# Optimization experiments

Hardware: AMD Instinct MI355X
Metric: run time of the kernel (lower is better)

The kernel has to match this reference:

```python
import jax, jax.numpy as jnp
import numpy as np

D = 1024  # in_features == latent_dim
EPS = 1e-5


def _layernorm(x, g, b):
    mu = jnp.mean(x, axis=-1, keepdims=True)
    var = jnp.mean(jnp.square(x - mu), axis=-1, keepdims=True)
    return (x - mu) * jax.lax.rsqrt(var + EPS) * g + b


def setup_inputs() -> dict:
    key = jax.random.key(0)
    ks = jax.random.split(key, 8)
    s = 1.0 / np.sqrt(D)
    return {
        "x": jax.random.normal(ks[0], (4, 4096, D), dtype=jnp.float32),
        "w_qkv": jax.random.uniform(ks[1], (3 * D, D), jnp.float32, -s, s),
        "w_o": jax.random.uniform(ks[2], (D, D), jnp.float32, -s, s),
        "w1": jax.random.uniform(ks[3], (D, D), jnp.float32, -s, s),
        "b1": jax.random.uniform(ks[4], (D,), jnp.float32, -s, s),
        "w2": jax.random.uniform(ks[5], (D, D), jnp.float32, -s, s),
        "b2": jax.random.uniform(ks[6], (D,), jnp.float32, -s, s),
        "ln1_g": jnp.ones((D,), jnp.float32),
        "ln1_b": jnp.zeros((D,), jnp.float32),
        "ln2_g": jnp.ones((D,), jnp.float32),
        "ln2_b": jnp.zeros((D,), jnp.float32),
    }


def reference(x, w_qkv, w_o, w1, b1, w2, b2, ln1_g, ln1_b, ln2_g, ln2_b):
    B, S, _ = x.shape
    scale = 1.0 / np.sqrt(D * 1)  # 1/sqrt(latent_dim * n_heads), n_heads=1
    qkv = jnp.einsum("bsd,ed->bse", x, w_qkv)            # [B,S,3D]
    qkv = qkv.reshape(B, S, 1, 3 * D).transpose(0, 2, 1, 3)  # [B,1,S,3D]
    q, k, v = jnp.split(qkv, 3, axis=-1)                  # each [B,1,S,D]
    logits = jnp.einsum("bhid,bhjd->bhij", q, k) * scale  # [B,1,S,S]
    # Faithful quirk: softmax over the HEAD axis (dim=1). With 1 head this
    # yields an all-ones attention matrix.
    attn = jax.nn.softmax(logits, axis=1)
    vals = jnp.einsum("bhij,bhjd->bhid", attn, v)         # [B,1,S,D]
    vals = vals.transpose(0, 2, 1, 3).reshape(B, S, D)
    attn_out = jnp.einsum("bsd,ed->bse", vals, w_o)
    # squeeze(-2) is a no-op for S>1
    x = _layernorm(x + attn_out, ln1_g, ln1_b)
    h = jax.nn.gelu(jnp.einsum("bsd,ed->bse", x, w1) + b1, approximate=False)
    mlp_out = jnp.einsum("bsd,ed->bse", h, w2) + b2
    return _layernorm(x + mlp_out, ln2_g, ln2_b)
```

## Files before the change

kernel.cpp:

```cpp
#include <hip/hip_runtime.h>
#include <hip/hip_bf16.h>

typedef __hip_bfloat16 bf16;
typedef __attribute__((ext_vector_type(8))) short short8;
typedef __attribute__((ext_vector_type(4))) float f32x4;

#define DDIM 1024
#define SEQ  4096
#define NB   4
#define MTOT (NB*SEQ)

static __device__ __forceinline__ unsigned short f2bf(float f) {
    __hip_bfloat16 h = __float2bfloat16(f);
    unsigned short u; __builtin_memcpy(&u, &h, 2); return u;
}
static __device__ __forceinline__ float bf2f(unsigned short u) {
    __hip_bfloat16 h; __builtin_memcpy(&h, &u, 2); return __bfloat162float(h);
}

__global__ __launch_bounds__(256) void cast_w_kernel(
    const float* __restrict__ w1, const float* __restrict__ w2,
    unsigned short* __restrict__ w1b, unsigned short* __restrict__ w2b)
{
    size_t idx = ((size_t)blockIdx.x*256 + threadIdx.x) * 4;
    float4 a = *(const float4*)(w1 + idx);
    ushort4 o; o.x=f2bf(a.x); o.y=f2bf(a.y); o.z=f2bf(a.z); o.w=f2bf(a.w);
    *(ushort4*)(w1b + idx) = o;
    float4 b = *(const float4*)(w2 + idx);
    o.x=f2bf(b.x); o.y=f2bf(b.y); o.z=f2bf(b.z); o.w=f2bf(b.w);
    *(ushort4*)(w2b + idx) = o;
}

__global__ __launch_bounds__(256) void colsum_partial_kernel(
    const float* __restrict__ x, float* __restrict__ partial)
{
    int d  = blockIdx.x*256 + threadIdx.x;
    int b  = blockIdx.y;
    int sl = blockIdx.z;
    const float* p = x + ((size_t)b*SEQ + (size_t)sl*128)*DDIM + d;
    float s = 0.f;
    #pragma unroll 4
    for (int i = 0; i < 128; ++i) s += p[(size_t)i*DDIM];
    partial[((size_t)sl*NB + b)*DDIM + d] = s;
}

__global__ __launch_bounds__(256) void colsum_reduce_kernel(
    const float* __restrict__ partial, float* __restrict__ xsum)
{
    int d = blockIdx.x*256 + threadIdx.x;
    int b = blockIdx.y;
    float s = 0.f;
    #pragma unroll
    for (int sl = 0; sl < 32; ++sl) s += partial[((size_t)sl*NB + b)*DDIM + d];
    xsum[b*DDIM + d] = s;
}

__global__ __launch_bounds__(256) void matvec_kernel(
    const float* __restrict__ W, const float* __restrict__ vin, float* __restrict__ vout)
{
    int b = blockIdx.y;
    int g = threadIdx.x >> 4;
    int t = threadIdx.x & 15;
    int e = blockIdx.x*16 + g;
    const float* w = W + (size_t)e*DDIM;
    const float* v = vin + b*DDIM;
    float s = 0.f;
    for (int k = t; k < DDIM; k += 16) s += w[k]*v[k];
    #pragma unroll
    for (int o = 8; o; o >>= 1) s += __shfl_down(s, o, 16);
    if (t == 0) vout[b*DDIM + e] = s;
}

__global__ __launch_bounds__(256) void ln1_kernel(
    const float* __restrict__ x, const float* __restrict__ avec,
    const float* __restrict__ g1, const float* __restrict__ b1,
    unsigned short* __restrict__ x1b)
{
    int row = blockIdx.x;
    int b   = row >> 12;
    int tid = threadIdx.x;
    const float4* xr = (const float4*)(x + (size_t)row*DDIM);
    const float4* av = (const float4*)(avec + (size_t)b*DDIM);
    float4 xv = xr[tid], a4 = av[tid];
    float y0 = xv.x+a4.x, y1 = xv.y+a4.y, y2 = xv.z+a4.z, y3 = xv.w+a4.w;
    float s  = y0+y1+y2+y3;
    float ss = y0*y0+y1*y1+y2*y2+y3*y3;
    #pragma unroll
    for (int o = 32; o; o >>= 1) { s += __shfl_down(s,o,64); ss += __shfl_down(ss,o,64); }
    __shared__ float red[8];
    if ((tid&63) == 0) { red[tid>>6] = s; red[4+(tid>>6)] = ss; }
    __syncthreads();
    float St = red[0]+red[1]+red[2]+red[3];
    float Sq = red[4]+red[5]+red[6]+red[7];
    float mu = St*(1.0f/DDIM);
    float rs = rsqrtf(Sq*(1.0f/DDIM) - mu*mu + 1e-5f);
    float4 g4 = ((const float4*)g1)[tid];
    float4 bb = ((const float4*)b1)[tid];
    ushort4 o;
    o.x = f2bf((y0-mu)*rs*g4.x + bb.x);
    o.y = f2bf((y1-mu)*rs*g4.y + bb.y);
    o.z = f2bf((y2-mu)*rs*g4.z + bb.z);
    o.w = f2bf((y3-mu)*rs*g4.w + bb.w);
    *(ushort4*)(x1b + (size_t)row*DDIM + tid*4) = o;
}

template<int MODE>
__global__ __launch_bounds__(256, 2) void gemm128_kernel(
    const bf16* __restrict__ A, const bf16* __restrict__ Bw,
    const float* __restrict__ bias, const unsigned short* __restrict__ resid,
    unsigned short* __restrict__ outb, float* __restrict__ outf)
{
    constexpr int K = 1024, N = 1024, BK = 64, NT = K / BK;
    __shared__ __align__(16) bf16 lds[2][2][128*BK];
    const int tid  = threadIdx.x;
    const int wave = tid >> 6, lane = tid & 63;

    int bid = blockIdx.x;
    int swz = (bid & 7) * 128 + (bid >> 3);
    const size_t bm = (size_t)(swz >> 3) * 128;
    const size_t bn = (size_t)(swz & 7) * 128;

    const int wm = wave >> 1;
    const int wn = wave & 1;

    const int srow = tid >> 3;
    const int skel = (((tid & 7) ^ ((tid >> 3) & 7)) << 3);

    const int frow = lane & 15;
    int foff[2];
    #pragma unroll
    for (int ks = 0; ks < 2; ++ks)
        foff[ks] = frow*128 + (((ks*4 + (lane >> 4)) ^ (lane & 7)) << 4);

    f32x4 acc[4][4] = {};
    const bf16* Ab = A  + bm * K;
    const bf16* Bb = Bw + bn * K;

    auto stage = [&](int b, int kt) {
        #pragma unroll
        for (int mat = 0; mat < 2; ++mat) {
            const bf16* src = (mat == 0 ? Ab : Bb);
            #pragma unroll
            for (int g = 0; g < 4; ++g) {
                int row = g*32 + srow;
                const bf16* gp = src + (size_t)row * K + kt*BK + skel;
                __builtin_amdgcn_global_load_lds(
                    (const __attribute__((address_space(1))) void*)gp,
                    (__attribute__((address_space(3))) void*)
                        ((char*)&lds[b][mat][0] + g*4096 + wave*1024),
                    16, 0, 0);
            }
        }
    };

    stage(0, 0);

    #pragma unroll 2
    for (int t = 0; t < NT; ++t) {
        const int cur = t & 1;
        if (t < NT-1) {
            stage(cur ^ 1, t + 1);
            asm volatile("s_waitcnt vmcnt(8)" ::: "memory");
        } else {
            asm volatile("s_waitcnt vmcnt(0)" ::: "memory");
        }
        __builtin_amdgcn_s_barrier();

        const char* LA = (const char*)&lds[cur][0][0] + wm*8192;
        const char* LB = (const char*)&lds[cur][1][0] + wn*8192;
        #pragma unroll
        for (int ks = 0; ks < 2; ++ks) {
            short8 af[4], bfr[4];
            #pragma unroll
            for (int m = 0; m < 4; ++m) af[m]  = *(const short8*)(LA + m*2048 + foff[ks]);
            #pragma unroll
            for (int n = 0; n < 4; ++n) bfr[n] = *(const short8*)(LB + n*2048 + foff[ks]);
            __builtin_amdgcn_s_setprio(1);
            #pragma unroll
            for (int m = 0; m < 4; ++m)
                #pragma unroll
                for (int n = 0; n < 4; ++n)
                    acc[m][n] = __builtin_amdgcn_mfma_f32_16x16x32_bf16(af[m], bfr[n], acc[m][n], 0, 0, 0);
            __builtin_amdgcn_s_setprio(0);
        }
        __builtin_amdgcn_s_barrier();
    }

    const int crow = (lane >> 4) * 4, ccol = lane & 15;
    #pragma unroll
    for (int n = 0; n < 4; ++n) {
        size_t col = bn + wn*64 + n*16 + ccol;
        float bv = bias[col];
        #pragma unroll
        for (int m = 0; m < 4; ++m) {
            #pragma unroll
            for (int r = 0; r < 4; ++r) {
                size_t row = bm + wm*64 + m*16 + crow + r;
                float v = acc[m][n][r] + bv;
                if (MODE == 1) {
                    float ge = 0.5f*v*(1.0f + erff(v*0.70710678118f));
                    outb[row*(size_t)N + col] = f2bf(ge);
                } else {
                    outf[row*(size_t)N + col] = v + bf2f(resid[row*(size_t)N + col]);
                }
            }
        }
    }
}

__global__ __launch_bounds__(256) void ln2_kernel(
    float* __restrict__ out, const float* __restrict__ g2, const float* __restrict__ b2)
{
    int row = blockIdx.x;
    int tid = threadIdx.x;
    float4* orow = (float4*)(out + (size_t)row*DDIM);
    float4 y = orow[tid];
    float s  = y.x+y.y+y.z+y.w;
    float ss = y.x*y.x+y.y*y.y+y.z*y.z+y.w*y.w;
    #pragma unroll
    for (int o = 32; o; o >>= 1) { s += __shfl_down(s,o,64); ss += __shfl_down(ss,o,64); }
    __shared__ float red[8];
    if ((tid&63) == 0) { red[tid>>6] = s; red[4+(tid>>6)] = ss; }
    __syncthreads();
    float St = red[0]+red[1]+red[2]+red[3];
    float Sq = red[4]+red[5]+red[6]+red[7];
    float mu = St*(1.0f/DDIM);
    float rs = rsqrtf(Sq*(1.0f/DDIM) - mu*mu + 1e-5f);
    float4 g4 = ((const float4*)g2)[tid];
    float4 bb = ((const float4*)b2)[tid];
    float4 n;
    n.x = (y.x-mu)*rs*g4.x + bb.x;
    n.y = (y.y-mu)*rs*g4.y + bb.y;
    n.z = (y.z-mu)*rs*g4.z + bb.z;
    n.w = (y.w-mu)*rs*g4.w + bb.w;
    orow[tid] = n;
}

extern "C" void kernel_launch(void* const* d_in, const int* in_sizes, int n_in,
                              void* d_out, int out_size, void* d_ws, size_t ws_size,
                              hipStream_t stream)
{
    const float* x     = (const float*)d_in[0];
    const float* w_qkv = (const float*)d_in[1];
    const float* w_o   = (const float*)d_in[2];
    const float* w1    = (const float*)d_in[3];
    const float* b1    = (const float*)d_in[4];
    const float* w2    = (const float*)d_in[5];
    const float* b2    = (const float*)d_in[6];
    const float* ln1g  = (const float*)d_in[7];
    const float* ln1b  = (const float*)d_in[8];
    const float* ln2g  = (const float*)d_in[9];
    const float* ln2b  = (const float*)d_in[10];
    float* out = (float*)d_out;
    char* ws = (char*)d_ws;

    unsigned short* x1b = (unsigned short*)(ws);
    unsigned short* hb  = (unsigned short*)(ws + 33554432);
    unsigned short* w1b = (unsigned short*)(ws + 67108864);
    unsigned short* w2b = (unsigned short*)(ws + 69206016);
    float* partial = (float*)(ws + 71303168);
    float* xsum    = (float*)(ws + 71827456);
    float* tvec    = (float*)(ws + 71843840);
    float* avec    = (float*)(ws + 71860224);

    cast_w_kernel<<<dim3(1024), 256, 0, stream>>>(w1, w2, w1b, w2b);
    colsum_partial_kernel<<<dim3(4, NB, 32), 256, 0, stream>>>(x, partial);
    colsum_reduce_kernel<<<dim3(4, NB), 256, 0, stream>>>(partial, xsum);
    matvec_kernel<<<dim3(64, NB), 256, 0, stream>>>(w_qkv + (size_t)2*DDIM*DDIM, xsum, tvec);
    matvec_kernel<<<dim3(64, NB), 256, 0, stream>>>(w_o, tvec, avec);
    ln1_kernel<<<dim3(MTOT), 256, 0, stream>>>(x, avec, ln1g, ln1b, x1b);
    gemm128_kernel<1><<<dim3(1024), 256, 0, stream>>>(
        (const bf16*)x1b, (const bf16*)w1b, b1, nullptr, hb, nullptr);
    gemm128_kernel<2><<<dim3(1024), 256, 0, stream>>>(
        (const bf16*)hb, (const bf16*)w2b, b2, x1b, nullptr, out);
    ln2_kernel<<<dim3(MTOT), 256, 0, stream>>>(out, ln2g, ln2b);
}
```

Baseline: 174.6 us.

## Pre-pack weights into MFMA fragment layout and load B directly to registers

The weight cast kernel now writes w1/w2 as bf16 in MFMA B-fragment order, so each lane can fetch its 16-byte fragment with one coalesced global load. The GEMM keeps only A in LDS through global_load_lds, and B fragments are double-buffered in registers and prefetched one k-step ahead. This halves LDS traffic and the LDS footprint and removes the B LDS reads. In exchange each wave loads its own B fragments, so B global and L2 traffic rises because the two wm waves duplicate them, and register pressure increases.

```diff
diff --git a/kernel.cpp b/kernel.cpp
--- a/kernel.cpp
+++ b/kernel.cpp
@@ -18,17 +18,24 @@
     __hip_bfloat16 h; __builtin_memcpy(&h, &u, 2); return __bfloat162float(h);
 }
 
-__global__ __launch_bounds__(256) void cast_w_kernel(
+__global__ __launch_bounds__(256) void pack_w_kernel(
     const float* __restrict__ w1, const float* __restrict__ w2,
-    unsigned short* __restrict__ w1b, unsigned short* __restrict__ w2b)
-{
-    size_t idx = ((size_t)blockIdx.x*256 + threadIdx.x) * 4;
-    float4 a = *(const float4*)(w1 + idx);
-    ushort4 o; o.x=f2bf(a.x); o.y=f2bf(a.y); o.z=f2bf(a.z); o.w=f2bf(a.w);
-    *(ushort4*)(w1b + idx) = o;
-    float4 b = *(const float4*)(w2 + idx);
-    o.x=f2bf(b.x); o.y=f2bf(b.y); o.z=f2bf(b.z); o.w=f2bf(b.w);
-    *(ushort4*)(w2b + idx) = o;
+    short8* __restrict__ w1p, short8* __restrict__ w2p)
+{
+    int gid  = blockIdx.x*256 + threadIdx.x;
+    int m    = gid >> 17;
+    int id   = gid & 131071;
+    int frag = id >> 6, lane = id & 63;
+    int ntile = frag >> 5, kt32 = frag & 31;
+    int n = ntile*16 + (lane & 15);
+    int k = kt32*32 + (lane >> 4)*8;
+    const float* src = (m ? w2 : w1) + (size_t)n*DDIM + k;
+    float4 a = *(const float4*)src;
+    float4 b = *(const float4*)(src + 4);
+    short8 o;
+    o[0]=(short)f2bf(a.x); o[1]=(short)f2bf(a.y); o[2]=(short)f2bf(a.z); o[3]=(short)f2bf(a.w);
+    o[4]=(short)f2bf(b.x); o[5]=(short)f2bf(b.y); o[6]=(short)f2bf(b.z); o[7]=(short)f2bf(b.w);
+    (m ? w2p : w1p)[id] = o;
 }
 
 __global__ __launch_bounds__(256) void colsum_partial_kernel(
@@ -105,13 +112,13 @@
 }
 
 template<int MODE>
-__global__ __launch_bounds__(256, 2) void gemm128_kernel(
-    const bf16* __restrict__ A, const bf16* __restrict__ Bw,
+__global__ __launch_bounds__(256, 2) void gemm_bp_kernel(
+    const bf16* __restrict__ A, const short8* __restrict__ Bp,
     const float* __restrict__ bias, const unsigned short* __restrict__ resid,
     unsigned short* __restrict__ outb, float* __restrict__ outf)
 {
     constexpr int K = 1024, N = 1024, BK = 64, NT = K / BK;
-    __shared__ __align__(16) bf16 lds[2][2][128*BK];
+    __shared__ __align__(16) bf16 lds[2][128*BK];
     const int tid  = threadIdx.x;
     const int wave = tid >> 6, lane = tid & 63;
 
@@ -126,64 +133,75 @@
     const int srow = tid >> 3;
     const int skel = (((tid & 7) ^ ((tid >> 3) & 7)) << 3);
 
-    const int frow = lane & 15;
+    const int fr = lane & 15;
+    const int fs = lane >> 4;
     int foff[2];
     #pragma unroll
     for (int ks = 0; ks < 2; ++ks)
-        foff[ks] = frow*128 + (((ks*4 + (lane >> 4)) ^ (lane & 7)) << 4);
+        foff[ks] = fr*128 + (((ks*4 + fs) ^ (fr & 7)) << 4);
+
+    const bf16* Ab = A + bm * K;
+    const int nt0 = (int)(bn >> 4) + wn*4;
+
+    auto stageA = [&](int b, int kt) {
+        #pragma unroll
+        for (int g = 0; g < 4; ++g) {
+            const bf16* gp = Ab + (size_t)(g*32 + srow) * K + kt*BK + skel;
+            __builtin_amdgcn_global_load_lds(
+                (const __attribute__((address_space(1))) void*)gp,
+                (__attribute__((address_space(3))) void*)
+                    ((char*)&lds[b][0] + g*4096 + wave*1024),
+                16, 0, 0);
+        }
+    };
+    auto loadB = [&](int kt, short8* bf_) {
+        #pragma unroll
+        for (int kk = 0; kk < 2; ++kk)
+            #pragma unroll
+            for (int nf = 0; nf < 4; ++nf)
+                bf_[kk*4 + nf] = Bp[((nt0 + nf)*32 + kt*2 + kk)*64 + lane];
+    };
 
     f32x4 acc[4][4] = {};
-    const bf16* Ab = A  + bm * K;
-    const bf16* Bb = Bw + bn * K;
-
-    auto stage = [&](int b, int kt) {
-        #pragma unroll
-        for (int mat = 0; mat < 2; ++mat) {
-            const bf16* src = (mat == 0 ? Ab : Bb);
-            #pragma unroll
-            for (int g = 0; g < 4; ++g) {
-                int row = g*32 + srow;
-                const bf16* gp = src + (size_t)row * K + kt*BK + skel;
-                __builtin_amdgcn_global_load_lds(
-                    (const __attribute__((address_space(1))) void*)gp,
-                    (__attribute__((address_space(3))) void*)
-                        ((char*)&lds[b][mat][0] + g*4096 + wave*1024),
-                    16, 0, 0);
-            }
-        }
-    };
-
-    stage(0, 0);
-
-    #pragma unroll 2
-    for (int t = 0; t < NT; ++t) {
-        const int cur = t & 1;
+    short8 bcur[8], bnxt[8];
+
+    stageA(0, 0);
+    loadB(0, bcur);
+
+    auto iter = [&](int t, short8* bc, short8* bn_) {
         if (t < NT-1) {
-            stage(cur ^ 1, t + 1);
-            asm volatile("s_waitcnt vmcnt(8)" ::: "memory");
+            stageA((t+1) & 1, t+1);
+            asm volatile("s_waitcnt vmcnt(4)" ::: "memory");
         } else {
             asm volatile("s_waitcnt vmcnt(0)" ::: "memory");
         }
         __builtin_amdgcn_s_barrier();
-
-        const char* LA = (const char*)&lds[cur][0][0] + wm*8192;
-        const char* LB = (const char*)&lds[cur][1][0] + wn*8192;
+        if (t < NT-1) {
+            loadB(t+1, bn_);
+            asm volatile("" ::: "memory");
+        }
+        const char* LA = (const char*)&lds[t & 1][0] + wm*8192;
         #pragma unroll
         for (int ks = 0; ks < 2; ++ks) {
-            short8 af[4], bfr[4];
-            #pragma unroll
-            for (int m = 0; m < 4; ++m) af[m]  = *(const short8*)(LA + m*2048 + foff[ks]);
-            #pragma unroll
-            for (int n = 0; n < 4; ++n) bfr[n] = *(const short8*)(LB + n*2048 + foff[ks]);
+            short8 af[4];
+            #pragma unroll
+            for (int m = 0; m < 4; ++m) af[m] = *(const short8*)(LA + m*2048 + foff[ks]);
             __builtin_amdgcn_s_setprio(1);
             #pragma unroll
             for (int m = 0; m < 4; ++m)
                 #pragma unroll
                 for (int n = 0; n < 4; ++n)
-                    acc[m][n] = __builtin_amdgcn_mfma_f32_16x16x32_bf16(af[m], bfr[n], acc[m][n], 0, 0, 0);
+                    acc[m][n] = __builtin_amdgcn_mfma_f32_16x16x32_bf16(
+                        af[m], bc[ks*4 + n], acc[m][n], 0, 0, 0);
             __builtin_amdgcn_s_setprio(0);
         }
         __builtin_amdgcn_s_barrier();
+    };
+
+    #pragma unroll
+    for (int t = 0; t < NT; t += 2) {
+        iter(t,   bcur, bnxt);
+        iter(t+1, bnxt, bcur);
     }
 
     const int crow = (lane >> 4) * 4, ccol = lane & 15;
@@ -256,22 +274,22 @@
 
     unsigned short* x1b = (unsigned short*)(ws);
     unsigned short* hb  = (unsigned short*)(ws + 33554432);
-    unsigned short* w1b = (unsigned short*)(ws + 67108864);
-    unsigned short* w2b = (unsigned short*)(ws + 69206016);
+    short8* w1p = (short8*)(ws + 67108864);
+    short8* w2p = (short8*)(ws + 69206016);
     float* partial = (float*)(ws + 71303168);
     float* xsum    = (float*)(ws + 71827456);
     float* tvec    = (float*)(ws + 71843840);
     float* avec    = (float*)(ws + 71860224);
 
-    cast_w_kernel<<<dim3(1024), 256, 0, stream>>>(w1, w2, w1b, w2b);
+    pack_w_kernel<<<dim3(1024), 256, 0, stream>>>(w1, w2, w1p, w2p);
     colsum_partial_kernel<<<dim3(4, NB, 32), 256, 0, stream>>>(x, partial);
     colsum_reduce_kernel<<<dim3(4, NB), 256, 0, stream>>>(partial, xsum);
     matvec_kernel<<<dim3(64, NB), 256, 0, stream>>>(w_qkv + (size_t)2*DDIM*DDIM, xsum, tvec);
     matvec_kernel<<<dim3(64, NB), 256, 0, stream>>>(w_o, tvec, avec);
     ln1_kernel<<<dim3(MTOT), 256, 0, stream>>>(x, avec, ln1g, ln1b, x1b);
-    gemm128_kernel<1><<<dim3(1024), 256, 0, stream>>>(
-        (const bf16*)x1b, (const bf16*)w1b, b1, nullptr, hb, nullptr);
-    gemm128_kernel<2><<<dim3(1024), 256, 0, stream>>>(
-        (const bf16*)hb, (const bf16*)w2b, b2, x1b, nullptr, out);
+    gemm_bp_kernel<1><<<dim3(1024), 256, 0, stream>>>(
+        (const bf16*)x1b, w1p, b1, nullptr, hb, nullptr);
+    gemm_bp_kernel<2><<<dim3(1024), 256, 0, stream>>>(
+        (const bf16*)hb, w2p, b2, x1b, nullptr, out);
     ln2_kernel<<<dim3(MTOT), 256, 0, stream>>>(out, ln2g, ln2b);
 }
```

After: 187.2 us. 7.2% more time.

## Fuse LN2 statistics into second GEMM epilogue and add single-buffered first GEMM

Applied to the files above, without the earlier changes.

The second GEMM's epilogue now writes the residual sum in bf16 in place over x1b and computes per-row partial sum and sum-of-squares through shuffles and LDS. It writes these partials to a small buffer, so the final LayerNorm kernel reads bf16 values plus 8 partials instead of re-reading and reducing an fp32 row. The first GEMM is replaced by a single-buffered BK=32 kernel with 3 blocks per CU that synchronises every k-step. This cuts fp32 traffic and a reduction pass, at the cost of rounding the pre-LN2 sum to bf16 and computing variance as E[x²]−mu² from bf16-rounded values. The lnpart buffer reuses the w1b region, which is safe because the first GEMM has finished reading it by then.

```diff
diff --git a/kernel.cpp b/kernel.cpp
--- a/kernel.cpp
+++ b/kernel.cpp
@@ -104,11 +104,84 @@
     *(ushort4*)(x1b + (size_t)row*DDIM + tid*4) = o;
 }
 
-template<int MODE>
-__global__ __launch_bounds__(256, 2) void gemm128_kernel(
+__global__ __launch_bounds__(256, 3) void gemm_s32_kernel(
     const bf16* __restrict__ A, const bf16* __restrict__ Bw,
-    const float* __restrict__ bias, const unsigned short* __restrict__ resid,
-    unsigned short* __restrict__ outb, float* __restrict__ outf)
+    const float* __restrict__ bias, unsigned short* __restrict__ outb)
+{
+    constexpr int K = 1024, N = 1024, BK = 32;
+    __shared__ __align__(16) bf16 As[128*BK];
+    __shared__ __align__(16) bf16 Bs[128*BK];
+    const int tid  = threadIdx.x;
+    const int wave = tid >> 6, lane = tid & 63;
+
+    int bid = blockIdx.x;
+    int swz = (bid & 7) * 128 + (bid >> 3);
+    const size_t bm = (size_t)(swz >> 3) * 128;
+    const size_t bn = (size_t)(swz & 7) * 128;
+
+    const int wr = (wave >> 1) * 64, wc = (wave & 1) * 64;
+    const int fr = lane & 15, fs = lane >> 4;
+
+    const int srow = lane >> 2;
+    const int sk   = (((lane & 3) ^ ((lane >> 3) & 3)) << 3);
+
+    const int swo = (fs ^ ((fr >> 1) & 3)) << 4;
+
+    f32x4 acc[4][4] = {};
+    const bf16* Ab = A  + bm * K;
+    const bf16* Bb = Bw + bn * K;
+
+    for (int kt = 0; kt < K; kt += BK) {
+        #pragma unroll
+        for (int c = 0; c < 2; ++c) {
+            int chunk = c*4 + wave;
+            const bf16* ga = Ab + (size_t)(chunk*16 + srow)*K + kt + sk;
+            const bf16* gb = Bb + (size_t)(chunk*16 + srow)*K + kt + sk;
+            __builtin_amdgcn_global_load_lds(
+                (const __attribute__((address_space(1))) void*)ga,
+                (__attribute__((address_space(3))) void*)((char*)As + chunk*1024), 16, 0, 0);
+            __builtin_amdgcn_global_load_lds(
+                (const __attribute__((address_space(1))) void*)gb,
+                (__attribute__((address_space(3))) void*)((char*)Bs + chunk*1024), 16, 0, 0);
+        }
+        __syncthreads();
+        short8 af[4], bfr[4];
+        #pragma unroll
+        for (int m = 0; m < 4; ++m) af[m]  = *(const short8*)((char*)As + (wr + m*16 + fr)*64 + swo);
+        #pragma unroll
+        for (int n = 0; n < 4; ++n) bfr[n] = *(const short8*)((char*)Bs + (wc + n*16 + fr)*64 + swo);
+        __builtin_amdgcn_s_setprio(1);
+        #pragma unroll
+        for (int m = 0; m < 4; ++m)
+            #pragma unroll
+            for (int n = 0; n < 4; ++n)
+                acc[m][n] = __builtin_amdgcn_mfma_f32_16x16x32_bf16(af[m], bfr[n], acc[m][n], 0, 0, 0);
+        __builtin_amdgcn_s_setprio(0);
+        __syncthreads();
+    }
+
+    const int crow = fs * 4, ccol = fr;
+    #pragma unroll
+    for (int n = 0; n < 4; ++n) {
+        size_t col = bn + wc + n*16 + ccol;
+        float bv = bias[col];
+        #pragma unroll
+        for (int m = 0; m < 4; ++m) {
+            #pragma unroll
+            for (int r = 0; r < 4; ++r) {
+                size_t row = bm + wr + m*16 + crow + r;
+                float v = acc[m][n][r] + bv;
+                float ge = 0.5f*v*(1.0f + erff(v*0.70710678118f));
+                outb[row*(size_t)N + col] = f2bf(ge);
+            }
+        }
+    }
+}
+
+__global__ __launch_bounds__(256, 2) void gemm2_kernel(
+    const bf16* __restrict__ A, const bf16* __restrict__ Bw,
+    const float* __restrict__ bias, unsigned short* __restrict__ xy,
+    float2* __restrict__ part)
 {
     constexpr int K = 1024, N = 1024, BK = 64, NT = K / BK;
     __shared__ __align__(16) bf16 lds[2][2][128*BK];
@@ -126,11 +199,12 @@
     const int srow = tid >> 3;
     const int skel = (((tid & 7) ^ ((tid >> 3) & 7)) << 3);
 
-    const int frow = lane & 15;
+    const int fr = lane & 15;
+    const int fs = lane >> 4;
     int foff[2];
     #pragma unroll
     for (int ks = 0; ks < 2; ++ks)
-        foff[ks] = frow*128 + (((ks*4 + (lane >> 4)) ^ (lane & 7)) << 4);
+        foff[ks] = fr*128 + (((ks*4 + fs) ^ (fr & 7)) << 4);
 
     f32x4 acc[4][4] = {};
     const bf16* Ab = A  + bm * K;
@@ -180,60 +254,86 @@
             for (int m = 0; m < 4; ++m)
                 #pragma unroll
                 for (int n = 0; n < 4; ++n)
-                    acc[m][n] = __builtin_amdgcn_mfma_f32_16x16x32_bf16(af[m], bfr[n], acc[m][n], 0, 0, 0);
+                    acc[m][n] = __builtin_amdgcn_mfma_f32_16x16x32_bf16(
+                        af[m], bfr[n], acc[m][n], 0, 0, 0);
             __builtin_amdgcn_s_setprio(0);
         }
         __builtin_amdgcn_s_barrier();
     }
 
-    const int crow = (lane >> 4) * 4, ccol = lane & 15;
+    float vs[4][4] = {}, vq[4][4] = {};
     #pragma unroll
     for (int n = 0; n < 4; ++n) {
-        size_t col = bn + wn*64 + n*16 + ccol;
+        size_t col = bn + wn*64 + n*16 + fr;
         float bv = bias[col];
         #pragma unroll
         for (int m = 0; m < 4; ++m) {
             #pragma unroll
             for (int r = 0; r < 4; ++r) {
-                size_t row = bm + wm*64 + m*16 + crow + r;
-                float v = acc[m][n][r] + bv;
-                if (MODE == 1) {
-                    float ge = 0.5f*v*(1.0f + erff(v*0.70710678118f));
-                    outb[row*(size_t)N + col] = f2bf(ge);
-                } else {
-                    outf[row*(size_t)N + col] = v + bf2f(resid[row*(size_t)N + col]);
-                }
-            }
-        }
-    }
-}
-
-__global__ __launch_bounds__(256) void ln2_kernel(
-    float* __restrict__ out, const float* __restrict__ g2, const float* __restrict__ b2)
+                size_t row = bm + wm*64 + m*16 + fs*4 + r;
+                size_t idx = row*(size_t)N + col;
+                float v = acc[m][n][r] + bv + bf2f(xy[idx]);
+                unsigned short qb = f2bf(v);
+                xy[idx] = qb;
+                float vv = bf2f(qb);
+                vs[m][r] += vv;
+                vq[m][r] += vv*vv;
+            }
+        }
+    }
+    #pragma unroll
+    for (int o = 1; o < 16; o <<= 1) {
+        #pragma unroll
+        for (int m = 0; m < 4; ++m)
+            #pragma unroll
+            for (int r = 0; r < 4; ++r) {
+                vs[m][r] += __shfl_xor(vs[m][r], o);
+                vq[m][r] += __shfl_xor(vq[m][r], o);
+            }
+    }
+    float* lred = (float*)&lds[0][0][0];
+    if (fr == 0) {
+        #pragma unroll
+        for (int m = 0; m < 4; ++m)
+            #pragma unroll
+            for (int r = 0; r < 4; ++r) {
+                int rl = wm*64 + m*16 + fs*4 + r;
+                lred[(wn*128 + rl)*2]     = vs[m][r];
+                lred[(wn*128 + rl)*2 + 1] = vq[m][r];
+            }
+    }
+    __syncthreads();
+    if (tid < 128) {
+        float s  = lred[tid*2]       + lred[(128 + tid)*2];
+        float sq = lred[tid*2 + 1]   + lred[(128 + tid)*2 + 1];
+        part[(bm + tid)*8 + (bn >> 7)] = make_float2(s, sq);
+    }
+}
+
+__global__ __launch_bounds__(256) void ln2_apply_kernel(
+    const unsigned short* __restrict__ yb, const float2* __restrict__ part,
+    const float* __restrict__ g2, const float* __restrict__ b2,
+    float* __restrict__ out)
 {
     int row = blockIdx.x;
     int tid = threadIdx.x;
-    float4* orow = (float4*)(out + (size_t)row*DDIM);
-    float4 y = orow[tid];
-    float s  = y.x+y.y+y.z+y.w;
-    float ss = y.x*y.x+y.y*y.y+y.z*y.z+y.w*y.w;
-    #pragma unroll
-    for (int o = 32; o; o >>= 1) { s += __shfl_down(s,o,64); ss += __shfl_down(ss,o,64); }
-    __shared__ float red[8];
-    if ((tid&63) == 0) { red[tid>>6] = s; red[4+(tid>>6)] = ss; }
-    __syncthreads();
-    float St = red[0]+red[1]+red[2]+red[3];
-    float Sq = red[4]+red[5]+red[6]+red[7];
-    float mu = St*(1.0f/DDIM);
-    float rs = rsqrtf(Sq*(1.0f/DDIM) - mu*mu + 1e-5f);
+    float s = 0.f, sq = 0.f;
+    #pragma unroll
+    for (int i = 0; i < 8; ++i) {
+        float2 p = part[(size_t)row*8 + i];
+        s += p.x; sq += p.y;
+    }
+    float mu = s * (1.0f/DDIM);
+    float rs = rsqrtf(sq * (1.0f/DDIM) - mu*mu + 1e-5f);
+    ushort4 yv = *(const ushort4*)(yb + (size_t)row*DDIM + tid*4);
     float4 g4 = ((const float4*)g2)[tid];
     float4 bb = ((const float4*)b2)[tid];
-    float4 n;
-    n.x = (y.x-mu)*rs*g4.x + bb.x;
-    n.y = (y.y-mu)*rs*g4.y + bb.y;
-    n.z = (y.z-mu)*rs*g4.z + bb.z;
-    n.w = (y.w-mu)*rs*g4.w + bb.w;
-    orow[tid] = n;
+    float4 o;
+    o.x = (bf2f(yv.x) - mu)*rs*g4.x + bb.x;
+    o.y = (bf2f(yv.y) - mu)*rs*g4.y + bb.y;
+    o.z = (bf2f(yv.z) - mu)*rs*g4.z + bb.z;
+    o.w = (bf2f(yv.w) - mu)*rs*g4.w + bb.w;
+    ((float4*)(out + (size_t)row*DDIM))[tid] = o;
 }
 
 extern "C" void kernel_launch(void* const* d_in, const int* in_sizes, int n_in,
@@ -262,6 +362,7 @@
     float* xsum    = (float*)(ws + 71827456);
     float* tvec    = (float*)(ws + 71843840);
     float* avec    = (float*)(ws + 71860224);
+    float2* lnpart = (float2*)(ws + 67108864);
 
     cast_w_kernel<<<dim3(1024), 256, 0, stream>>>(w1, w2, w1b, w2b);
     colsum_partial_kernel<<<dim3(4, NB, 32), 256, 0, stream>>>(x, partial);
@@ -269,9 +370,9 @@
     matvec_kernel<<<dim3(64, NB), 256, 0, stream>>>(w_qkv + (size_t)2*DDIM*DDIM, xsum, tvec);
     matvec_kernel<<<dim3(64, NB), 256, 0, stream>>>(w_o, tvec, avec);
     ln1_kernel<<<dim3(MTOT), 256, 0, stream>>>(x, avec, ln1g, ln1b, x1b);
-    gemm128_kernel<1><<<dim3(1024), 256, 0, stream>>>(
-        (const bf16*)x1b, (const bf16*)w1b, b1, nullptr, hb, nullptr);
-    gemm128_kernel<2><<<dim3(1024), 256, 0, stream>>>(
-        (const bf16*)hb, (const bf16*)w2b, b2, x1b, nullptr, out);
-    ln2_kernel<<<dim3(MTOT), 256, 0, stream>>>(out, ln2g, ln2b);
-}
+    gemm_s32_kernel<<<dim3(1024), 256, 0, stream>>>(
+        (const bf16*)x1b, (const bf16*)w1b, b1, hb);
+    gemm2_kernel<<<dim3(1024), 256, 0, stream>>>(
+        (const bf16*)hb, (const bf16*)w2b, b2, x1b, lnpart);
+    ln2_apply_kernel<<<dim3(MTOT), 256, 0, stream>>>(x1b, lnpart, ln2g, ln2b, out);
+}
```

After: 174.8 us. About the same (+0.1%).
